# Kernel optimization log

Measured on AMD Instinct MI355X. Metric: run time of the kernel, lower is better.

Reference implementation:

```python
import jax, jax.numpy as jnp
import numpy as np

B, V_IN, V_OUT, F_IN, F_OUT, N_CP = 100000, 128, 128, 512, 512, 16
DIM_H = max(V_IN, V_OUT)  # hidden_vectors=None -> max(dim_vectors_in, dim_vectors_out)
EPS = 1e-8


def setup_inputs() -> dict:
    key = jax.random.key(0)
    ks = jax.random.split(key, 9)
    u = lambda k, shape, scale: jax.random.uniform(k, shape, jnp.float32, -scale, scale)
    wh_k = 1.0 / np.sqrt(V_IN).astype(np.float32)
    wu_k = 1.0 / np.sqrt(DIM_H + N_CP).astype(np.float32)
    f_in = DIM_H + N_CP + F_IN  # 656
    kf = 1.0 / np.sqrt(f_in).astype(np.float32)
    kg = 1.0 / np.sqrt(F_OUT).astype(np.float32)
    return {
        "feats": jax.random.normal(ks[0], (B, F_IN), jnp.float32),
        "vectors": jax.random.normal(ks[1], (B, V_IN, 3), jnp.float32),
        "Wh": u(ks[2], (V_IN, DIM_H), wh_k),
        "Wcp": u(ks[3], (V_IN, 2 * N_CP), wh_k),
        "Wu": u(ks[4], (DIM_H + N_CP, V_OUT), wu_k),
        "Wf": u(ks[5], (f_in, F_OUT), kf),      # torch Linear weight, stored (in,out)
        "bf": u(ks[6], (F_OUT,), kf),
        "Wg": u(ks[7], (F_OUT, V_OUT), kg),
        "bg": u(ks[8], (V_OUT,), kg),
    }


def reference(feats, vectors, Wh, Wcp, Wu, Wf, bf, Wg, bg):
    # vectors: [b, v_in, 3]; mix vector channels (matmul acts per xyz component c)
    Vh = jnp.einsum('bvc,vh->bhc', vectors, Wh)            # [b, dim_h, 3]
    # cross-product features
    Vcp = jnp.einsum('bvc,vp->bpc', vectors, Wcp)          # [b, 2*n_cp, 3]
    cp = jnp.cross(Vcp[:, :N_CP], Vcp[:, N_CP:])           # [b, n_cp, 3]
    Vh = jnp.concatenate([Vh, cp], axis=1)                 # [b, dim_h+n_cp, 3]
    Vu = jnp.einsum('bkc,ko->boc', Vh, Wu)                 # [b, v_out, 3]
    # clamped L2 norm over xyz
    sh = jnp.sqrt(jnp.maximum(jnp.sum(Vh * Vh, axis=-1), EPS))  # [b, dim_h+n_cp]
    s = jnp.concatenate([feats, sh], axis=1)               # [b, dim_h+n_cp+f_in]
    feats_out = jax.nn.silu(s @ Wf + bf)                   # [b, f_out]
    gating = feats_out @ Wg + bg                           # [b, v_out]
    vectors_out = jax.nn.sigmoid(gating)[..., None] * Vu   # [b, v_out, 3]
    return feats_out, vectors_out
```

## Files before the change

### kernel.cpp

```cpp
#include <hip/hip_runtime.h>

#define BATCH 100000
#define M3 300000
#define VECBASE 51200000
#define KP 704

typedef float fl4  __attribute__((ext_vector_type(4)));
typedef float f32x4 __attribute__((ext_vector_type(4)));
typedef short s16x4 __attribute__((ext_vector_type(4)));
typedef short s16x8 __attribute__((ext_vector_type(8)));

__device__ __forceinline__ short f2bf(float f) {
  unsigned int u = __float_as_uint(f);
  u += 0x7fffu + ((u >> 16) & 1u);
  return (short)(u >> 16);
}
__device__ __forceinline__ float bf2f(short s) {
  return __uint_as_float(((unsigned int)(unsigned short)s) << 16);
}
__device__ __forceinline__ s16x8 pack8(fl4 a, fl4 b) {
  s16x8 o;
  o[0] = f2bf(a[0]); o[1] = f2bf(a[1]); o[2] = f2bf(a[2]); o[3] = f2bf(a[3]);
  o[4] = f2bf(b[0]); o[5] = f2bf(b[1]); o[6] = f2bf(b[2]); o[7] = f2bf(b[3]);
  return o;
}
__device__ __forceinline__ void glds16(const void* g, void* l) {
  __builtin_amdgcn_global_load_lds((const __attribute__((address_space(1))) void*)g,
                                   (__attribute__((address_space(3))) void*)l, 16, 0, 0);
}
#define WAITBAR(N) asm volatile("s_waitcnt vmcnt(" #N ")\ns_barrier" ::: "memory")
#define RAWBAR()   asm volatile("s_barrier" ::: "memory")

__global__ __launch_bounds__(256) void prep_w(
    const float* __restrict__ feats, const float* __restrict__ Wh,
    const float* __restrict__ Wcp, const float* __restrict__ Wu,
    const float* __restrict__ Wf, const float* __restrict__ Wg,
    short* __restrict__ Ab, short* __restrict__ WB1, short* __restrict__ WuTp,
    short* __restrict__ WfT, short* __restrict__ WgT) {
  const int tid = blockIdx.x * 256 + threadIdx.x;
  const int stride = gridDim.x * 256;
  for (int i = tid; i < 6400000; i += stride) {
    int b = i >> 6, kk = (i & 63) * 8;
    fl4 v0 = *reinterpret_cast<const fl4*>(&feats[(size_t)b * 512 + kk]);
    fl4 v1 = *reinterpret_cast<const fl4*>(&feats[(size_t)b * 512 + kk + 4]);
    *(s16x8*)&Ab[(size_t)b * KP + kk] = pack8(v0, v1);
  }
  for (int gid = tid; gid < 466944; gid += stride) {
    if (gid < 20480) {
      int n = gid >> 7, k = gid & 127;
      WB1[gid] = f2bf(n < 128 ? Wh[k * 128 + n] : Wcp[k * 32 + (n - 128)]);
    } else if (gid < 40960) {
      int i = gid - 20480;
      int o = i / 160, k = i - o * 160;
      WuTp[i] = k < 144 ? f2bf(Wu[k * 128 + o]) : (short)0;
    } else if (gid < 401408) {
      int i = gid - 40960;
      int n = i / KP, k = i - n * KP;
      WfT[i] = k < 656 ? f2bf(Wf[k * 512 + n]) : (short)0;
    } else {
      int i = gid - 401408;
      int n = i >> 9, k = i & 511;
      WgT[i] = f2bf(Wg[k * 128 + n]);
    }
  }
}

__global__ __launch_bounds__(256) void geo_fused(
    const float* __restrict__ vecs, const short* __restrict__ WB1,
    const short* __restrict__ WuTp, short* __restrict__ Ab,
    short* __restrict__ Vub) {
  __shared__ __align__(16) short U[96 * 168];
  const int t = threadIdx.x;
  const int b0 = blockIdx.x * 32;
  const int row0 = blockIdx.x * 96;

#pragma unroll
  for (int it = 0; it < 4; ++it) {
    int fi = (it * 256 + t) * 12;
    int bl = fi / 384;
    int rem = fi - bl * 384;
    int v0 = rem / 3;
    const float* p = &vecs[(size_t)(b0 + bl) * 384 + rem];
    fl4 x = *(const fl4*)p, y = *(const fl4*)(p + 4), z = *(const fl4*)(p + 8);
    float vc[3][4] = {{x[0], x[3], y[2], z[1]},
                      {x[1], y[0], y[3], z[2]},
                      {x[2], y[1], z[0], z[3]}};
#pragma unroll
    for (int c = 0; c < 3; ++c) {
      int row = bl * 3 + c;
      s16x4 q;
#pragma unroll
      for (int e = 0; e < 4; ++e) q[e] = f2bf(vc[c][e]);
      int off = (row << 8) + (v0 << 1);
      *(s16x4*)((char*)U + (off ^ ((row & 7) << 4))) = q;
    }
  }
  __syncthreads();

  const int lane = t & 63, wv = t >> 6;
  const int wr = wv >> 1, wc = wv & 1;
  const int lr = lane & 15, lk = lane >> 4;

  {
    f32x4 acc[3][5];
#pragma unroll
    for (int i = 0; i < 3; ++i)
#pragma unroll
      for (int j = 0; j < 5; ++j) acc[i][j] = (f32x4){0.f, 0.f, 0.f, 0.f};
#pragma unroll
    for (int kk = 0; kk < 4; ++kk) {
      s16x8 af[3], bq[5];
#pragma unroll
      for (int mi = 0; mi < 3; ++mi) {
        int row = wr * 48 + mi * 16 + lr;
        int off = (row << 8) + (kk << 6) + (lk << 4);
        af[mi] = *(const s16x8*)((const char*)U + (off ^ ((row & 7) << 4)));
      }
#pragma unroll
      for (int ni = 0; ni < 5; ++ni)
        bq[ni] = *reinterpret_cast<const s16x8*>(
            &WB1[(wc * 80 + ni * 16 + lr) * 128 + (kk << 5) + (lk << 3)]);
      __builtin_amdgcn_s_setprio(1);
#pragma unroll
      for (int mi = 0; mi < 3; ++mi)
#pragma unroll
        for (int ni = 0; ni < 5; ++ni)
          acc[mi][ni] = __builtin_amdgcn_mfma_f32_16x16x32_bf16(af[mi], bq[ni], acc[mi][ni], 0, 0, 0);
      __builtin_amdgcn_s_setprio(0);
    }
    __syncthreads();
#pragma unroll
    for (int mi = 0; mi < 3; ++mi)
#pragma unroll
      for (int ni = 0; ni < 5; ++ni) {
        int col = wc * 80 + ni * 16 + lr;
#pragma unroll
        for (int r = 0; r < 4; ++r) {
          int row = wr * 48 + mi * 16 + lk * 4 + r;
          U[row * 168 + col] = f2bf(acc[mi][ni][r]);
        }
      }
  }
  __syncthreads();

  {
    int bl = t >> 3, pj = t & 7;
    int gb = b0 + bl;
    float shcp[2];
#pragma unroll
    for (int q = 0; q < 2; ++q) {
      int p = pj * 2 + q;
      float ax = bf2f(U[(bl * 3 + 0) * 168 + 128 + p]);
      float ay = bf2f(U[(bl * 3 + 1) * 168 + 128 + p]);
      float az = bf2f(U[(bl * 3 + 2) * 168 + 128 + p]);
      float bx = bf2f(U[(bl * 3 + 0) * 168 + 144 + p]);
      float by = bf2f(U[(bl * 3 + 1) * 168 + 144 + p]);
      float bz = bf2f(U[(bl * 3 + 2) * 168 + 144 + p]);
      float cx = ay * bz - az * by;
      float cy = az * bx - ax * bz;
      float cz = ax * by - ay * bx;
      U[(bl * 3 + 0) * 168 + 128 + p] = f2bf(cx);
      U[(bl * 3 + 1) * 168 + 128 + p] = f2bf(cy);
      U[(bl * 3 + 2) * 168 + 128 + p] = f2bf(cz);
      U[(bl * 3 + 0) * 168 + 144 + p] = 0;
      U[(bl * 3 + 1) * 168 + 144 + p] = 0;
      U[(bl * 3 + 2) * 168 + 144 + p] = 0;
      shcp[q] = sqrtf(fmaxf(cx * cx + cy * cy + cz * cz, 1e-8f));
    }
    Ab[(size_t)gb * KP + 640 + pj * 2]     = f2bf(shcp[0]);
    Ab[(size_t)gb * KP + 640 + pj * 2 + 1] = f2bf(shcp[1]);
#pragma unroll
    for (int z = 0; z < 6; ++z)
      Ab[(size_t)gb * KP + 656 + pj * 6 + z] = 0;
  }
  {
    int bl = t >> 3, kq = t & 7;
    int gb = b0 + bl;
#pragma unroll
    for (int j = 0; j < 2; ++j) {
      int k = kq * 16 + j * 8;
      s16x8 r0 = *(const s16x8*)&U[(bl * 3 + 0) * 168 + k];
      s16x8 r1 = *(const s16x8*)&U[(bl * 3 + 1) * 168 + k];
      s16x8 r2 = *(const s16x8*)&U[(bl * 3 + 2) * 168 + k];
      s16x8 o;
#pragma unroll
      for (int e = 0; e < 8; ++e) {
        float x = bf2f(r0[e]), y = bf2f(r1[e]), z = bf2f(r2[e]);
        o[e] = f2bf(sqrtf(fmaxf(x * x + y * y + z * z, 1e-8f)));
      }
      *(s16x8*)&Ab[(size_t)gb * KP + 512 + k] = o;
    }
  }
  __syncthreads();

  {
    f32x4 acc2[3][4];
#pragma unroll
    for (int i = 0; i < 3; ++i)
#pragma unroll
      for (int j = 0; j < 4; ++j) acc2[i][j] = (f32x4){0.f, 0.f, 0.f, 0.f};
#pragma unroll
    for (int kk = 0; kk < 5; ++kk) {
      s16x8 af[3], bq[4];
#pragma unroll
      for (int mi = 0; mi < 3; ++mi) {
        int row = wr * 48 + mi * 16 + lr;
        af[mi] = *(const s16x8*)&U[row * 168 + (kk << 5) + (lk << 3)];
      }
#pragma unroll
      for (int ni = 0; ni < 4; ++ni)
        bq[ni] = *reinterpret_cast<const s16x8*>(
            &WuTp[(wc * 64 + ni * 16 + lr) * 160 + (kk << 5) + (lk << 3)]);
      __builtin_amdgcn_s_setprio(1);
#pragma unroll
      for (int mi = 0; mi < 3; ++mi)
#pragma unroll
        for (int ni = 0; ni < 4; ++ni)
          acc2[mi][ni] = __builtin_amdgcn_mfma_f32_16x16x32_bf16(af[mi], bq[ni], acc2[mi][ni], 0, 0, 0);
      __builtin_amdgcn_s_setprio(0);
    }
#pragma unroll
    for (int mi = 0; mi < 3; ++mi)
#pragma unroll
      for (int ni = 0; ni < 4; ++ni) {
        int col = wc * 64 + ni * 16 + lr;
#pragma unroll
        for (int r = 0; r < 4; ++r) {
          int row = row0 + wr * 48 + mi * 16 + lk * 4 + r;
          Vub[(size_t)row * 128 + col] = f2bf(acc2[mi][ni][r]);
        }
      }
  }
}

__global__ __launch_bounds__(512, 4) void gemm_feats(
    const short* __restrict__ Ab, const short* __restrict__ WfT,
    const float* __restrict__ bfv, float* __restrict__ out,
    short* __restrict__ fob) {
  const int bid = blockIdx.x;
  const int xcd = bid & 7, bi = bid >> 3;
  const int swz = (xcd < 4 ? xcd * 196 : 784 + (xcd - 4) * 195) + bi;
  const int mt = swz >> 1, nt = swz & 1;
  const int row0 = mt << 7, n0 = nt << 8;
  const int t = threadIdx.x;
  const int lane = t & 63, wv = t >> 6;
  const int wr = wv >> 2, wc = wv & 3;
  const int lr = lane & 15, lk = lane >> 4;

  __shared__ __align__(16) short As[2][128 * 32];
  __shared__ __align__(16) short Bs[2][256 * 32];

  const int arow = t >> 2, ach = t & 3;
  const short* srcA = &Ab[(size_t)min(row0 + arow, BATCH - 1) * KP +
                          ((ach ^ ((arow >> 1) & 3))) * 8];
  const int adof = t * 8;
  const short* srcB[2]; int bdof[2];
#pragma unroll
  for (int j = 0; j < 2; ++j) {
    int cid = j * 512 + t;
    int brow = cid >> 2, bch = cid & 3;
    srcB[j] = &WfT[(size_t)(n0 + brow) * KP + ((bch ^ ((brow >> 1) & 3))) * 8];
    bdof[j] = cid * 8;
  }

  f32x4 acc[4][4];
#pragma unroll
  for (int i = 0; i < 4; ++i)
#pragma unroll
    for (int j = 0; j < 4; ++j) acc[i][j] = (f32x4){0.f, 0.f, 0.f, 0.f};

  auto STAGE = [&](int buf, int ks) {
    const int k0 = ks << 5;
    glds16(srcA + k0, &As[buf][adof]);
    glds16(srcB[0] + k0, &Bs[buf][bdof[0]]);
    glds16(srcB[1] + k0, &Bs[buf][bdof[1]]);
  };
  auto COMPUTE = [&](int buf) {
    s16x8 af[4], bq[4];
#pragma unroll
    for (int mi = 0; mi < 4; ++mi) {
      int rw = wr * 64 + mi * 16 + lr;
      af[mi] = *(const s16x8*)&As[buf][rw * 32 + (lk ^ ((rw >> 1) & 3)) * 8];
    }
#pragma unroll
    for (int ni = 0; ni < 4; ++ni) {
      int rn = wc * 64 + ni * 16 + lr;
      bq[ni] = *(const s16x8*)&Bs[buf][rn * 32 + (lk ^ ((rn >> 1) & 3)) * 8];
    }
    __builtin_amdgcn_s_setprio(1);
#pragma unroll
    for (int mi = 0; mi < 4; ++mi)
#pragma unroll
      for (int ni = 0; ni < 4; ++ni)
        acc[mi][ni] = __builtin_amdgcn_mfma_f32_16x16x32_bf16(af[mi], bq[ni], acc[mi][ni], 0, 0, 0);
    __builtin_amdgcn_s_setprio(0);
  };

  STAGE(0, 0);
  STAGE(1, 1);
  for (int ks = 0; ks < 22; ++ks) {
    if (ks < 21) WAITBAR(3);
    else         WAITBAR(0);
    COMPUTE(ks & 1);
    RAWBAR();
    if (ks + 2 < 22) STAGE(ks & 1, ks + 2);
  }

  float* Ls = (float*)&As[0][0];
#pragma unroll
  for (int g = 0; g < 8; ++g) {
    __syncthreads();
    if (wr == (g >> 2)) {
      int mi = g & 3;
#pragma unroll
      for (int ni = 0; ni < 4; ++ni) {
        int colL = wc * 64 + ni * 16 + lr;
        float bb = bfv[n0 + colL];
#pragma unroll
        for (int rr = 0; rr < 4; ++rr) {
          float x = acc[mi][ni][rr] + bb;
          Ls[(lk * 4 + rr) * 256 + colL] = x / (1.f + __expf(-x));
        }
      }
    }
    __syncthreads();
    {
      int rowL = t >> 5, seg = t & 31;
      int grow = row0 + g * 16 + rowL;
      if (grow < BATCH) {
        const float* p = &Ls[rowL * 256 + seg * 8];
        fl4 a = *(const fl4*)p, b = *(const fl4*)(p + 4);
        float* po = &out[(size_t)grow * 512 + n0 + seg * 8];
        *(fl4*)po = a; *(fl4*)(po + 4) = b;
        *(s16x8*)&fob[(size_t)grow * 512 + n0 + seg * 8] = pack8(a, b);
      }
    }
  }
}

__global__ __launch_bounds__(512, 4) void gemm_gate(
    const short* __restrict__ fob, const short* __restrict__ WgT,
    const float* __restrict__ bg, const short* __restrict__ Vub,
    float* __restrict__ out) {
  const int bid = blockIdx.x;
  const int xcd = bid & 7, bi = bid >> 3;
  const int swz = (xcd < 7 ? xcd * 49 : 343 + (xcd - 7) * 48) + bi;
  const int row0 = swz << 8;
  const int t = threadIdx.x;
  const int lane = t & 63, wv = t >> 6;
  const int wr = wv >> 1, wc = wv & 1;
  const int lr = lane & 15, lk = lane >> 4;

  __shared__ __align__(16) short S[(256 + 128) * 64];
  short* As = S;
  short* Bs = S + 256 * 64;

  const short* srcA[4]; int adof[4];
#pragma unroll
  for (int j = 0; j < 4; ++j) {
    int cid = j * 512 + t;
    int row = cid >> 3, ch = cid & 7;
    srcA[j] = &fob[(size_t)min(row0 + row, BATCH - 1) * 512 + (ch ^ (row & 7)) * 8];
    adof[j] = cid * 8;
  }
  const short* srcB[2]; int bdof[2];
#pragma unroll
  for (int j = 0; j < 2; ++j) {
    int cid = j * 512 + t;
    int row = cid >> 3, ch = cid & 7;
    srcB[j] = &WgT[(size_t)row * 512 + (ch ^ (row & 7)) * 8];
    bdof[j] = cid * 8;
  }

  f32x4 acc[4][4];
#pragma unroll
  for (int i = 0; i < 4; ++i)
#pragma unroll
    for (int j = 0; j < 4; ++j) acc[i][j] = (f32x4){0.f, 0.f, 0.f, 0.f};

  for (int ks = 0; ks < 8; ++ks) {
    const int k0 = ks << 6;
    __syncthreads();
#pragma unroll
    for (int j = 0; j < 4; ++j) glds16(srcA[j] + k0, &As[adof[j]]);
    glds16(srcB[0] + k0, &Bs[bdof[0]]);
    glds16(srcB[1] + k0, &Bs[bdof[1]]);
    __syncthreads();
#pragma unroll
    for (int kk = 0; kk < 2; ++kk) {
      s16x8 af[4], bq[4];
#pragma unroll
      for (int mi = 0; mi < 4; ++mi) {
        int rw = wr * 64 + mi * 16 + lr;
        af[mi] = *(const s16x8*)&As[rw * 64 + (((kk << 2) + lk) ^ (rw & 7)) * 8];
      }
#pragma unroll
      for (int ni = 0; ni < 4; ++ni) {
        int rn = wc * 64 + ni * 16 + lr;
        bq[ni] = *(const s16x8*)&Bs[rn * 64 + (((kk << 2) + lk) ^ (rn & 7)) * 8];
      }
      __builtin_amdgcn_s_setprio(1);
#pragma unroll
      for (int mi = 0; mi < 4; ++mi)
#pragma unroll
        for (int ni = 0; ni < 4; ++ni)
          acc[mi][ni] = __builtin_amdgcn_mfma_f32_16x16x32_bf16(af[mi], bq[ni], acc[mi][ni], 0, 0, 0);
      __builtin_amdgcn_s_setprio(0);
    }
  }

#pragma unroll
  for (int ni = 0; ni < 4; ++ni) {
    int col = wc * 64 + ni * 16 + lr;
    float bb = bg[col];
#pragma unroll
    for (int mi = 0; mi < 4; ++mi) {
      int rbase = row0 + wr * 64 + mi * 16 + lk * 4;
#pragma unroll
      for (int rr = 0; rr < 4; ++rr) {
        int gr = rbase + rr;
        if (gr < BATCH) {
          float x = acc[mi][ni][rr] + bb;
          float gate = 1.f / (1.f + __expf(-x));
          size_t vb = (size_t)(3 * gr) * 128 + col;
          float* po = &out[VECBASE + ((size_t)gr * 128 + col) * 3];
          po[0] = gate * bf2f(Vub[vb]);
          po[1] = gate * bf2f(Vub[vb + 128]);
          po[2] = gate * bf2f(Vub[vb + 256]);
        }
      }
    }
  }
}

extern "C" void kernel_launch(void* const* d_in, const int* in_sizes, int n_in,
                              void* d_out, int out_size, void* d_ws, size_t ws_size,
                              hipStream_t stream) {
  const float* feats = (const float*)d_in[0];
  const float* vecs  = (const float*)d_in[1];
  const float* Wh    = (const float*)d_in[2];
  const float* Wcp   = (const float*)d_in[3];
  const float* Wu    = (const float*)d_in[4];
  const float* Wf    = (const float*)d_in[5];
  const float* bfv   = (const float*)d_in[6];
  const float* Wg    = (const float*)d_in[7];
  const float* bg    = (const float*)d_in[8];
  float* out = (float*)d_out;

  char* ws = (char*)d_ws;
  short* Ab   = (short*)ws;
  short* Vub  = (short*)(ws + 140800000);
  short* fob  = (short*)(ws + 217600000);
  short* WfT  = (short*)(ws + 320000000);
  short* WgT  = (short*)(ws + 320720896);
  short* WB1  = (short*)(ws + 320851968);
  short* WuTp = (short*)(ws + 320892928);

  hipLaunchKernelGGL(prep_w,     dim3(2048), dim3(256), 0, stream,
                     feats, Wh, Wcp, Wu, Wf, Wg, Ab, WB1, WuTp, WfT, WgT);
  hipLaunchKernelGGL(geo_fused,  dim3(3125), dim3(256), 0, stream,
                     vecs, WB1, WuTp, Ab, Vub);
  hipLaunchKernelGGL(gemm_feats, dim3(1564), dim3(512), 0, stream,
                     Ab, WfT, bfv, out, fob);
  hipLaunchKernelGGL(gemm_gate,  dim3(391),  dim3(512), 0, stream,
                     fob, WgT, bg, Vub, out);
}
```

Baseline: 435.7 us.

## Triple-buffer feats GEMM LDS and halve epilogue passes

The feats GEMM moves from two LDS stages to three in a single shared array. This lets the next stage's global-to-LDS loads start right after compute, without the extra barrier that kept a buffer from being overwritten while still being read. The epilogue now writes 32 rows per pass instead of 16, so there are 4 passes instead of 8 and half as many __syncthreads, and each thread stores 16 contiguous elements. The larger LDS footprint (about 74KB per block instead of about 49KB) may cut how many blocks fit on a CU.

```diff
diff --git a/kernel.cpp b/kernel.cpp
--- a/kernel.cpp
+++ b/kernel.cpp
@@ -29,7 +29,6 @@
                                    (__attribute__((address_space(3))) void*)l, 16, 0, 0);
 }
 #define WAITBAR(N) asm volatile("s_waitcnt vmcnt(" #N ")\ns_barrier" ::: "memory")
-#define RAWBAR()   asm volatile("s_barrier" ::: "memory")
 
 __global__ __launch_bounds__(256) void prep_w(
     const float* __restrict__ feats, const float* __restrict__ Wh,
@@ -247,8 +246,7 @@
   const int wr = wv >> 2, wc = wv & 3;
   const int lr = lane & 15, lk = lane >> 4;
 
-  __shared__ __align__(16) short As[2][128 * 32];
-  __shared__ __align__(16) short Bs[2][256 * 32];
+  __shared__ __align__(16) short S[3 * 128 * 32 + 3 * 256 * 32];
 
   const int arow = t >> 2, ach = t & 3;
   const short* srcA = &Ab[(size_t)min(row0 + arow, BATCH - 1) * KP +
@@ -271,21 +269,22 @@
 
   auto STAGE = [&](int buf, int ks) {
     const int k0 = ks << 5;
-    glds16(srcA + k0, &As[buf][adof]);
-    glds16(srcB[0] + k0, &Bs[buf][bdof[0]]);
-    glds16(srcB[1] + k0, &Bs[buf][bdof[1]]);
+    glds16(srcA + k0, &S[buf * 4096 + adof]);
+    glds16(srcB[0] + k0, &S[12288 + buf * 8192 + bdof[0]]);
+    glds16(srcB[1] + k0, &S[12288 + buf * 8192 + bdof[1]]);
   };
   auto COMPUTE = [&](int buf) {
+    const int ab = buf * 4096, bb = 12288 + buf * 8192;
     s16x8 af[4], bq[4];
 #pragma unroll
     for (int mi = 0; mi < 4; ++mi) {
       int rw = wr * 64 + mi * 16 + lr;
-      af[mi] = *(const s16x8*)&As[buf][rw * 32 + (lk ^ ((rw >> 1) & 3)) * 8];
+      af[mi] = *(const s16x8*)&S[ab + rw * 32 + (lk ^ ((rw >> 1) & 3)) * 8];
     }
 #pragma unroll
     for (int ni = 0; ni < 4; ++ni) {
       int rn = wc * 64 + ni * 16 + lr;
-      bq[ni] = *(const s16x8*)&Bs[buf][rn * 32 + (lk ^ ((rn >> 1) & 3)) * 8];
+      bq[ni] = *(const s16x8*)&S[bb + rn * 32 + (lk ^ ((rn >> 1) & 3)) * 8];
     }
     __builtin_amdgcn_s_setprio(1);
 #pragma unroll
@@ -301,38 +300,44 @@
   for (int ks = 0; ks < 22; ++ks) {
     if (ks < 21) WAITBAR(3);
     else         WAITBAR(0);
-    COMPUTE(ks & 1);
-    RAWBAR();
-    if (ks + 2 < 22) STAGE(ks & 1, ks + 2);
-  }
-
-  float* Ls = (float*)&As[0][0];
-#pragma unroll
-  for (int g = 0; g < 8; ++g) {
+    COMPUTE(ks % 3);
+    if (ks + 2 < 22) STAGE((ks + 2) % 3, ks + 2);
+  }
+
+  float* Ls = (float*)S;
+#pragma unroll
+  for (int g = 0; g < 4; ++g) {
     __syncthreads();
-    if (wr == (g >> 2)) {
-      int mi = g & 3;
-#pragma unroll
-      for (int ni = 0; ni < 4; ++ni) {
-        int colL = wc * 64 + ni * 16 + lr;
-        float bb = bfv[n0 + colL];
-#pragma unroll
-        for (int rr = 0; rr < 4; ++rr) {
-          float x = acc[mi][ni][rr] + bb;
-          Ls[(lk * 4 + rr) * 256 + colL] = x / (1.f + __expf(-x));
+    if (wr == (g >> 1)) {
+      int miB = (g & 1) * 2;
+#pragma unroll
+      for (int m2 = 0; m2 < 2; ++m2) {
+#pragma unroll
+        for (int ni = 0; ni < 4; ++ni) {
+          int colL = wc * 64 + ni * 16 + lr;
+          float bb = bfv[n0 + colL];
+#pragma unroll
+          for (int rr = 0; rr < 4; ++rr) {
+            int rowL = m2 * 16 + lk * 4 + rr;
+            float x = acc[miB + m2][ni][rr] + bb;
+            Ls[rowL * 256 + colL] = x / (1.f + __expf(-x));
+          }
         }
       }
     }
     __syncthreads();
     {
-      int rowL = t >> 5, seg = t & 31;
-      int grow = row0 + g * 16 + rowL;
+      int rowL = t >> 4, seg = t & 15;
+      int grow = row0 + g * 32 + rowL;
       if (grow < BATCH) {
-        const float* p = &Ls[rowL * 256 + seg * 8];
+        const float* p = &Ls[rowL * 256 + seg * 16];
         fl4 a = *(const fl4*)p, b = *(const fl4*)(p + 4);
-        float* po = &out[(size_t)grow * 512 + n0 + seg * 8];
-        *(fl4*)po = a; *(fl4*)(po + 4) = b;
-        *(s16x8*)&fob[(size_t)grow * 512 + n0 + seg * 8] = pack8(a, b);
+        fl4 c = *(const fl4*)(p + 8), d = *(const fl4*)(p + 12);
+        float* po = &out[(size_t)grow * 512 + n0 + seg * 16];
+        *(fl4*)po = a; *(fl4*)(po + 4) = b; *(fl4*)(po + 8) = c; *(fl4*)(po + 12) = d;
+        short* pf = &fob[(size_t)grow * 512 + n0 + seg * 16];
+        *(s16x8*)pf = pack8(a, b);
+        *(s16x8*)(pf + 8) = pack8(c, d);
       }
     }
   }
```

Result: slower. 451.9 us (+3.7%).

## Replace double-buffered K loop with single-buffer BK=64 synchronous staging in feats GEMM

Applied to the files above, without the earlier changes.

Drops the two-stage global_load_lds double buffer with hand-written vmcnt waits in gemm_feats. It uses a single shared buffer holding a 64-wide K slice, with an 8-way XOR swizzle and two full __syncthreads per iteration, so the loop runs 11 iterations instead of 22. This halves the barrier count and keeps LDS at the same size, which may help occupancy at 4 blocks per CU. In exchange, the copy of the next K slice no longer overlaps with the MFMA work inside a block, and the design relies on other resident blocks to hide load latency.

```diff
diff --git a/kernel.cpp b/kernel.cpp
--- a/kernel.cpp
+++ b/kernel.cpp
@@ -28,8 +28,6 @@
   __builtin_amdgcn_global_load_lds((const __attribute__((address_space(1))) void*)g,
                                    (__attribute__((address_space(3))) void*)l, 16, 0, 0);
 }
-#define WAITBAR(N) asm volatile("s_waitcnt vmcnt(" #N ")\ns_barrier" ::: "memory")
-#define RAWBAR()   asm volatile("s_barrier" ::: "memory")
 
 __global__ __launch_bounds__(256) void prep_w(
     const float* __restrict__ feats, const float* __restrict__ Wh,
@@ -247,19 +245,24 @@
   const int wr = wv >> 2, wc = wv & 3;
   const int lr = lane & 15, lk = lane >> 4;
 
-  __shared__ __align__(16) short As[2][128 * 32];
-  __shared__ __align__(16) short Bs[2][256 * 32];
-
-  const int arow = t >> 2, ach = t & 3;
-  const short* srcA = &Ab[(size_t)min(row0 + arow, BATCH - 1) * KP +
-                          ((ach ^ ((arow >> 1) & 3))) * 8];
-  const int adof = t * 8;
-  const short* srcB[2]; int bdof[2];
+  __shared__ __align__(16) short S[(128 + 256) * 64];
+  short* As = S;
+  short* Bs = S + 128 * 64;
+
+  const short* srcA[2]; int adof[2];
 #pragma unroll
   for (int j = 0; j < 2; ++j) {
     int cid = j * 512 + t;
-    int brow = cid >> 2, bch = cid & 3;
-    srcB[j] = &WfT[(size_t)(n0 + brow) * KP + ((bch ^ ((brow >> 1) & 3))) * 8];
+    int row = cid >> 3, ch = cid & 7;
+    srcA[j] = &Ab[(size_t)min(row0 + row, BATCH - 1) * KP + (ch ^ (row & 7)) * 8];
+    adof[j] = cid * 8;
+  }
+  const short* srcB[4]; int bdof[4];
+#pragma unroll
+  for (int j = 0; j < 4; ++j) {
+    int cid = j * 512 + t;
+    int row = cid >> 3, ch = cid & 7;
+    srcB[j] = &WfT[(size_t)(n0 + row) * KP + (ch ^ (row & 7)) * 8];
     bdof[j] = cid * 8;
   }
 
@@ -269,44 +272,38 @@
 #pragma unroll
     for (int j = 0; j < 4; ++j) acc[i][j] = (f32x4){0.f, 0.f, 0.f, 0.f};
 
-  auto STAGE = [&](int buf, int ks) {
-    const int k0 = ks << 5;
-    glds16(srcA + k0, &As[buf][adof]);
-    glds16(srcB[0] + k0, &Bs[buf][bdof[0]]);
-    glds16(srcB[1] + k0, &Bs[buf][bdof[1]]);
-  };
-  auto COMPUTE = [&](int buf) {
-    s16x8 af[4], bq[4];
-#pragma unroll
-    for (int mi = 0; mi < 4; ++mi) {
-      int rw = wr * 64 + mi * 16 + lr;
-      af[mi] = *(const s16x8*)&As[buf][rw * 32 + (lk ^ ((rw >> 1) & 3)) * 8];
-    }
-#pragma unroll
-    for (int ni = 0; ni < 4; ++ni) {
-      int rn = wc * 64 + ni * 16 + lr;
-      bq[ni] = *(const s16x8*)&Bs[buf][rn * 32 + (lk ^ ((rn >> 1) & 3)) * 8];
-    }
-    __builtin_amdgcn_s_setprio(1);
-#pragma unroll
-    for (int mi = 0; mi < 4; ++mi)
-#pragma unroll
-      for (int ni = 0; ni < 4; ++ni)
-        acc[mi][ni] = __builtin_amdgcn_mfma_f32_16x16x32_bf16(af[mi], bq[ni], acc[mi][ni], 0, 0, 0);
-    __builtin_amdgcn_s_setprio(0);
-  };
-
-  STAGE(0, 0);
-  STAGE(1, 1);
-  for (int ks = 0; ks < 22; ++ks) {
-    if (ks < 21) WAITBAR(3);
-    else         WAITBAR(0);
-    COMPUTE(ks & 1);
-    RAWBAR();
-    if (ks + 2 < 22) STAGE(ks & 1, ks + 2);
-  }
-
-  float* Ls = (float*)&As[0][0];
+  for (int ks = 0; ks < 11; ++ks) {
+    const int k0 = ks << 6;
+    __syncthreads();
+    glds16(srcA[0] + k0, &As[adof[0]]);
+    glds16(srcA[1] + k0, &As[adof[1]]);
+#pragma unroll
+    for (int j = 0; j < 4; ++j) glds16(srcB[j] + k0, &Bs[bdof[j]]);
+    __syncthreads();
+#pragma unroll
+    for (int kk = 0; kk < 2; ++kk) {
+      s16x8 af[4], bq[4];
+#pragma unroll
+      for (int mi = 0; mi < 4; ++mi) {
+        int rw = wr * 64 + mi * 16 + lr;
+        af[mi] = *(const s16x8*)&As[rw * 64 + (((kk << 2) + lk) ^ (rw & 7)) * 8];
+      }
+#pragma unroll
+      for (int ni = 0; ni < 4; ++ni) {
+        int rn = wc * 64 + ni * 16 + lr;
+        bq[ni] = *(const s16x8*)&Bs[rn * 64 + (((kk << 2) + lk) ^ (rn & 7)) * 8];
+      }
+      __builtin_amdgcn_s_setprio(1);
+#pragma unroll
+      for (int mi = 0; mi < 4; ++mi)
+#pragma unroll
+        for (int ni = 0; ni < 4; ++ni)
+          acc[mi][ni] = __builtin_amdgcn_mfma_f32_16x16x32_bf16(af[mi], bq[ni], acc[mi][ni], 0, 0, 0);
+      __builtin_amdgcn_s_setprio(0);
+    }
+  }
+
+  float* Ls = (float*)S;
 #pragma unroll
   for (int g = 0; g < 8; ++g) {
     __syncthreads();
```

Measured after the change: 427.6 us. About the same (-1.9%).
